# Performance work log

Hardware: AMD Instinct MI355X
Metric: run time of the kernel (lower is better)

## Reference

```python
import jax, jax.numpy as jnp
import numpy as np
from jax import lax

IMG = 256   # model img_size
O = 7       # adaptive pool output size (out_size)
R = 32      # number of ROIs
B = 8       # batch
CF = 32     # UNet output channels
FOUT = 512  # fc out_features


def _conv(x, w, b):
    y = lax.conv_general_dilated(x, w, (1, 1), 'SAME',
                                 dimension_numbers=('NCHW', 'OIHW', 'NCHW'))
    return y + b[None, :, None, None]


def _pool(x):
    return lax.reduce_window(x, -jnp.inf, lax.max, (1, 1, 2, 2), (1, 1, 2, 2), 'VALID')


def _up(x):
    return jnp.repeat(jnp.repeat(x, 2, axis=2), 2, axis=3)


def _unet(x, p):
    r = jax.nn.relu
    e1 = r(_conv(r(_conv(x, p['e1w1'], p['e1b1'])), p['e1w2'], p['e1b2']))          # [B,32,H,W]
    e2 = r(_conv(r(_conv(_pool(e1), p['e2w1'], p['e2b1'])), p['e2w2'], p['e2b2']))  # [B,64,H/2,W/2]
    bo = r(_conv(r(_conv(_pool(e2), p['bw1'], p['bb1'])), p['bw2'], p['bb2']))      # [B,128,H/4,W/4]
    u2 = r(_conv(_up(bo), p['u2w'], p['u2b']))                                      # [B,64,H/2,W/2]
    d2 = r(_conv(r(_conv(jnp.concatenate([u2, e2], 1), p['d2w1'], p['d2b1'])), p['d2w2'], p['d2b2']))
    u1 = r(_conv(_up(d2), p['u1w'], p['u1b']))                                      # [B,32,H,W]
    d1 = r(_conv(r(_conv(jnp.concatenate([u1, e1], 1), p['d1w1'], p['d1b1'])), p['d1w2'], p['d1b2']))
    return _conv(d1, p['fw'], p['fb'])                                              # [B,CF,H,W]


def _adaptive_pool(ii, boxes):
    # Exact F.adaptive_avg_pool2d bins via an integral image.
    # ii: [B,C,H+1,W+1] (zero-padded 2D cumsum); boxes: [R,4] int (x1,y1,x2,y2).
    i = jnp.arange(O)
    h = boxes[:, 3] - boxes[:, 1]
    w = boxes[:, 2] - boxes[:, 0]
    sy = boxes[:, 1:2] + (i[None, :] * h[:, None]) // O            # floor(i*h/O)
    ey = boxes[:, 1:2] + ((i[None, :] + 1) * h[:, None] + O - 1) // O  # ceil((i+1)*h/O)
    sx = boxes[:, 0:1] + (i[None, :] * w[:, None]) // O
    ex = boxes[:, 0:1] + ((i[None, :] + 1) * w[:, None] + O - 1) // O
    yA, yB = sy[:, :, None], ey[:, :, None]   # [R,O,1]
    xA, xB = sx[:, None, :], ex[:, None, :]   # [R,1,O]
    s = ii[:, :, yB, xB] - ii[:, :, yA, xB] - ii[:, :, yB, xA] + ii[:, :, yA, xA]  # [B,C,R,O,O]
    area = ((ey - sy)[:, :, None] * (ex - sx)[:, None, :]).astype(ii.dtype)        # [R,O,O]
    return s / area[None, None]


def _forward(x, rois, p):
    H, W = x.shape[2], x.shape[3]
    xs, ys = IMG // H, IMG // W  # matches torch: x_scale, y_scale = img_size//m, img_size//n
    boxes = rois // jnp.array([xs, ys, xs, ys], dtype=rois.dtype)
    f = _unet(x, p)                                   # [B,CF,H,W]
    ii = jnp.pad(jnp.cumsum(jnp.cumsum(f, axis=2), axis=3),
                 ((0, 0), (0, 0), (1, 0), (1, 0)))    # integral image [B,CF,H+1,W+1]
    rp = _adaptive_pool(ii, boxes)                    # [B,CF,R,O,O]
    roi_feat = jnp.transpose(rp, (0, 2, 1, 3, 4)).reshape(x.shape[0], boxes.shape[0] * f.shape[1], O, O)
    gbox = jnp.array([[0, 0, W, H]], dtype=boxes.dtype)
    gpool = _adaptive_pool(ii, gbox)[:, :, 0]         # [B,CF,O,O]
    out = jnp.concatenate([gpool, roi_feat], axis=1)  # [B,(R+1)*CF,O,O]
    out = out.reshape(out.shape[0], out.shape[1], O * O)
    return jnp.einsum('bnk,fk->bnf', out, p['fcw']) + p['fcb']


_PNAMES = ['e1w1','e1b1','e1w2','e1b2','e2w1','e2b1','e2w2','e2b2','bw1','bb1','bw2','bb2',
           'u2w','u2b','d2w1','d2b1','d2w2','d2b2','u1w','u1b','d1w1','d1b1','d1w2','d1b2',
           'fw','fb','fcw','fcb']


def setup_inputs() -> dict:
    key = jax.random.key(0)
    ks = jax.random.split(key, 32)

    def w(k, shape):
        fan = int(np.prod(shape[1:]))
        return jax.random.normal(k, shape, jnp.float32) * np.sqrt(2.0 / fan)

    d = {}
    d['x'] = jax.random.normal(ks[0], (B, 3, IMG, IMG), jnp.float32)
    xy1 = jax.random.randint(ks[1], (R, 2), 0, 192)
    wh = jax.random.randint(ks[2], (R, 2), 16, 64)
    d['rois'] = jnp.concatenate([xy1, xy1 + wh], axis=1).astype(jnp.int32)  # (x1,y1,x2,y2)

    shapes = {'e1w1': (32, 3, 3, 3), 'e1w2': (32, 32, 3, 3),
              'e2w1': (64, 32, 3, 3), 'e2w2': (64, 64, 3, 3),
              'bw1': (128, 64, 3, 3), 'bw2': (128, 128, 3, 3),
              'u2w': (64, 128, 3, 3),
              'd2w1': (64, 128, 3, 3), 'd2w2': (64, 64, 3, 3),
              'u1w': (32, 64, 3, 3),
              'd1w1': (32, 64, 3, 3), 'd1w2': (32, 32, 3, 3),
              'fw': (CF, 32, 1, 1),
              'fcw': (FOUT, O * O)}
    i = 3
    for n, s in shapes.items():
        d[n] = w(ks[i], s); i += 1
        bn = n.replace('w', 'b', 1) if 'w' in n else n
        d[bn] = jnp.zeros((s[0],), jnp.float32)
    d['fcb'] = jnp.zeros((FOUT,), jnp.float32)
    return d


def reference(x, rois, e1w1, e1b1, e1w2, e1b2, e2w1, e2b1, e2w2, e2b2,
              bw1, bb1, bw2, bb2, u2w, u2b, d2w1, d2b1, d2w2, d2b2,
              u1w, u1b, d1w1, d1b1, d1w2, d1b2, fw, fb, fcw, fcb):
    p = dict(e1w1=e1w1, e1b1=e1b1, e1w2=e1w2, e1b2=e1b2, e2w1=e2w1, e2b1=e2b1,
             e2w2=e2w2, e2b2=e2b2, bw1=bw1, bb1=bb1, bw2=bw2, bb2=bb2,
             u2w=u2w, u2b=u2b, d2w1=d2w1, d2b1=d2b1, d2w2=d2w2, d2b2=d2b2,
             u1w=u1w, u1b=u1b, d1w1=d1w1, d1b1=d1b1, d1w2=d1w2, d1b2=d1b2,
             fw=fw, fb=fb, fcw=fcw, fcb=fcb)
    return _forward(x, rois, p)
```

## Files before the change

### kernel.cpp

```cpp
#include <hip/hip_runtime.h>

typedef _Float16 half8 __attribute__((ext_vector_type(8)));
typedef float f32x4 __attribute__((ext_vector_type(4)));
typedef float f32x16 __attribute__((ext_vector_type(16)));

__device__ __forceinline__ unsigned short f2h(float f) {
    _Float16 h = (_Float16)f;
    return __builtin_bit_cast(unsigned short, h);
}
__device__ __forceinline__ float h2f(unsigned short u) {
    return (float)__builtin_bit_cast(_Float16, u);
}

__device__ __forceinline__ void lds_load16(const uint4* g, uint4* l) {
    __builtin_amdgcn_global_load_lds(
        (const __attribute__((address_space(1))) unsigned int*)g,
        (__attribute__((address_space(3))) unsigned int*)l, 16, 0, 0);
}

#define IIROW 260
#define IIPLANE 66824

__global__ void wprep_k(const float* __restrict__ src, unsigned short* __restrict__ dst,
                        int Cout, int Cin, int total)
{
    int t = blockIdx.x * 256 + threadIdx.x;
    if (t >= total) return;
    int j = t & 7; int r = t >> 3;
    int co = r % Cout; r /= Cout;
    int oct = r & 3; r >>= 2;
    int pos = r % 9; int ck = r / 9;
    int ci = ck * 32 + oct * 8 + j;
    dst[t] = f2h(src[((size_t)co * Cin + ci) * 9 + pos]);
}

__global__ void w1prep_k(const float* __restrict__ src, unsigned short* __restrict__ dst)
{
    int t = blockIdx.x * 256 + threadIdx.x;
    if (t >= 4096) return;
    int j = t & 7, co = (t >> 3) & 31, koct = t >> 8;
    dst[t] = f2h(src[co * 32 + koct * 8 + j]);
}

__global__ void fct_k(const float* __restrict__ src, float* __restrict__ dst)
{
    int t = blockIdx.x * 256 + threadIdx.x;
    if (t >= 49 * 512) return;
    int k = t >> 9, f = t & 511;
    dst[t] = src[f * 49 + k];
}

template<int BM, int TW, int TH, int LW, int UP>
__global__ __launch_bounds__(256, 2) void convm4_k(
    const uint4* __restrict__ in1, int C1g,
    const uint4* __restrict__ in2, int C2g,
    const uint4* __restrict__ wt,
    const float* __restrict__ bias,
    unsigned short* __restrict__ out,
    int Cout, int relu, const uint4* __restrict__ zp)
{
    constexpr int NM = BM / 16;
    constexpr int NN = (TW * TH) / 64;
    constexpr int CG = TW / 16;
    constexpr int RQ = NN / CG;
    static_assert(RQ == 2, "row-reuse layout needs 2 rows/wave");
    constexpr int Wf = 1 << LW, Hf = Wf;
    constexpr int WC = TW + 2, HR = TH + 2;
    constexpr int IN_GR = 4 * HR * WC;
    constexpr int LTW = (TW == 64) ? 6 : 5;
    constexpr int sH = UP ? (Hf >> 1) : Hf;
    constexpr int sW = UP ? (Wf >> 1) : Wf;
    __shared__ uint4 smem[IN_GR + 36 * BM];

    const int tid = threadIdx.x;
    const int lane = tid & 63, wv = tid >> 6;
    const int ng = Cout / BM;
    const int b = blockIdx.z / ng, cg = blockIdx.z % ng;
    const int x0 = blockIdx.x * TW, y0 = blockIdx.y * TH;
    const int NCK = (C1g + C2g) / 4;

    f32x4 acc[NM][NN];
#pragma unroll
    for (int m = 0; m < NM; ++m)
#pragma unroll
        for (int n = 0; n < NN; ++n) acc[m][n] = (f32x4){0.f, 0.f, 0.f, 0.f};

    const int l15 = lane & 15, l4 = lane >> 4;
    const int laneB = l4 * HR * WC + l15;
    const int laneA = l4 * BM + l15;

    for (int ck = 0; ck < NCK; ++ck) {
        if (ck) __syncthreads();
        {
            const uint4* src; int cg0, srcCg;
            if (ck * 4 < C1g) { src = in1; cg0 = ck * 4; srcCg = C1g; }
            else              { src = in2; cg0 = ck * 4 - C1g; srcCg = C2g; }
            for (int i = tid; i < IN_GR; i += 256) {
                int oct = i / (HR * WC);
                int rem = i - oct * (HR * WC);
                int row = rem / WC;
                int col = rem - row * WC;
                int gy = y0 + row - 1, gx = x0 + col - 1;
                int sy = UP ? (gy >> 1) : gy, sx = UP ? (gx >> 1) : gx;
                const uint4* ga = ((unsigned)gy < (unsigned)Hf && (unsigned)gx < (unsigned)Wf)
                    ? src + ((((size_t)b * sH + sy) * sW + sx) * srcCg + cg0 + oct)
                    : zp + (i & 63);
                lds_load16(ga, &smem[i]);
            }
        }
        {
            const uint4* wck = wt + (size_t)ck * 36 * Cout + (size_t)cg * BM;
            for (int i = tid; i < 36 * BM; i += 256) {
                int seg = i / BM, col = i - seg * BM;
                lds_load16(wck + seg * Cout + col, &smem[IN_GR + i]);
            }
        }
        __syncthreads();
        const half8* sB = (const half8*)smem;
        const half8* sA = (const half8*)(smem + IN_GR);
#pragma unroll
        for (int dc = 0; dc < 3; ++dc) {
            half8 br[RQ + 2][CG];
#pragma unroll
            for (int r = 0; r < RQ + 2; ++r)
#pragma unroll
                for (int c2 = 0; c2 < CG; ++c2)
                    br[r][c2] = sB[(wv * RQ + r) * WC + c2 * 16 + dc + laneB];
#pragma unroll
            for (int dr = 0; dr < 3; ++dr) {
                half8 af[NM];
#pragma unroll
                for (int m = 0; m < NM; ++m)
                    af[m] = sA[(dr * 3 + dc) * 4 * BM + m * 16 + laneA];
#pragma unroll
                for (int m = 0; m < NM; ++m)
#pragma unroll
                    for (int rq = 0; rq < RQ; ++rq)
#pragma unroll
                        for (int c2 = 0; c2 < CG; ++c2)
                            acc[m][rq * CG + c2] = __builtin_amdgcn_mfma_f32_16x16x32_f16(
                                af[m], br[rq + dr][c2], acc[m][rq * CG + c2], 0, 0, 0);
            }
        }
    }

#pragma unroll
    for (int m = 0; m < NM; ++m) {
        const int co0 = cg * BM + m * 16 + l4 * 4;
        const float4 bs = *(const float4*)(bias + co0);
#pragma unroll
        for (int n = 0; n < NN; ++n) {
            const int pix = wv * (NN * 16) + n * 16 + l15;
            const int y = y0 + (pix >> LTW), x = x0 + (pix & (TW - 1));
            float v0 = acc[m][n][0] + bs.x;
            float v1 = acc[m][n][1] + bs.y;
            float v2 = acc[m][n][2] + bs.z;
            float v3 = acc[m][n][3] + bs.w;
            if (relu) {
                v0 = fmaxf(v0, 0.f); v1 = fmaxf(v1, 0.f);
                v2 = fmaxf(v2, 0.f); v3 = fmaxf(v3, 0.f);
            }
            uint2 pk;
            pk.x = (unsigned)f2h(v0) | ((unsigned)f2h(v1) << 16);
            pk.y = (unsigned)f2h(v2) | ((unsigned)f2h(v3) << 16);
            *(uint2*)(out + (((size_t)b * Hf + y) * Wf + x) * Cout + co0) = pk;
        }
    }
}

__global__ __launch_bounds__(256) void conv0_k(
    const float* __restrict__ in, const float* __restrict__ w,
    const float* __restrict__ bias, unsigned short* __restrict__ out)
{
    __shared__ float s_in[3][18][18];
    const int tx = threadIdx.x, ty = threadIdx.y;
    const int tid = ty * 16 + tx;
    const int b = blockIdx.z >> 2;
    const int coBase = (blockIdx.z & 3) * 8;
    const int bx = blockIdx.x * 16, by = blockIdx.y * 16;

    for (int i = tid; i < 3 * 18 * 18; i += 256) {
        int cc = i / 324, r = i % 324;
        int ly = r / 18, lx = r % 18;
        int gy = by + ly - 1, gx = bx + lx - 1;
        float v = 0.f;
        if ((unsigned)gy < 256u && (unsigned)gx < 256u)
            v = in[(((size_t)(b * 3 + cc)) << 16) + (gy << 8) + gx];
        ((float*)s_in)[i] = v;
    }
    __syncthreads();
    float acc[8];
#pragma unroll
    for (int k = 0; k < 8; ++k) acc[k] = 0.f;
    for (int cc = 0; cc < 3; ++cc) {
        float v[9];
#pragma unroll
        for (int dh = 0; dh < 3; ++dh)
#pragma unroll
            for (int dw = 0; dw < 3; ++dw)
                v[dh * 3 + dw] = s_in[cc][ty + dh][tx + dw];
        const float* wp = w + ((size_t)coBase * 3 + cc) * 9;
#pragma unroll
        for (int k = 0; k < 8; ++k) {
            const float* wk = wp + (size_t)k * 27;
            float a = acc[k];
#pragma unroll
            for (int j = 0; j < 9; ++j) a = fmaf(v[j], wk[j], a);
            acc[k] = a;
        }
    }
    const int h = by + ty, ww = bx + tx;
    unsigned short* op = out + (((size_t)(b * 256 + h)) * 256 + ww) * 32 + coBase;
#pragma unroll
    for (int k = 0; k < 8; ++k)
        op[k] = f2h(fmaxf(acc[k] + bias[coBase + k], 0.f));
}

__global__ void poolh_k(const uint4* __restrict__ in, uint4* __restrict__ out,
                        int Ho, int Wo, int C8, int total)
{
    int i = blockIdx.x * 256 + threadIdx.x;
    if (i >= total) return;
    int oct = i % C8; int p = i / C8;
    int x = p % Wo; p /= Wo;
    int y = p % Ho; int b = p / Ho;
    const int H = Ho * 2, W = Wo * 2;
    size_t g = (((size_t)b * H + 2 * y) * W + 2 * x) * C8 + oct;
    uint4 v00 = in[g], v01 = in[g + C8];
    uint4 v10 = in[g + (size_t)W * C8], v11 = in[g + (size_t)W * C8 + C8];
    const unsigned short* a0 = (const unsigned short*)&v00;
    const unsigned short* a1 = (const unsigned short*)&v01;
    const unsigned short* a2 = (const unsigned short*)&v10;
    const unsigned short* a3 = (const unsigned short*)&v11;
    uint4 res; unsigned short* rp = (unsigned short*)&res;
#pragma unroll
    for (int j = 0; j < 8; ++j)
        rp[j] = f2h(fmaxf(fmaxf(h2f(a0[j]), h2f(a1[j])), fmaxf(h2f(a2[j]), h2f(a3[j]))));
    out[(((size_t)b * Ho + y) * Wo + x) * C8 + oct] = res;
}

__global__ __launch_bounds__(256) void rowprep_k(
    const uint4* __restrict__ in, const uint4* __restrict__ w16,
    const float* __restrict__ bias, float* __restrict__ ii)
{
    __shared__ uint4 sIn[1024];
    __shared__ uint4 sW[128];
    __shared__ float sout[32][256];
    __shared__ float sb[32];
    const int tid = threadIdx.x;
    const int lane = tid & 63, wv = tid >> 6;
    const int l31 = lane & 31, l5 = lane >> 5;
    const int y = blockIdx.x, b = blockIdx.y;

    const uint4* ip = in + (((size_t)b * 256 + y) * 256) * 4;
#pragma unroll
    for (int it = 0; it < 4; ++it)
        lds_load16(ip + tid + it * 256, &sIn[tid + it * 256]);
    if (tid < 128) lds_load16(w16 + tid, &sW[tid]);
    if (tid < 32) sb[tid] = bias[tid];
    __syncthreads();

    const half8* hW = (const half8*)sW;
    const half8* hIn = (const half8*)sIn;
    half8 af0 = hW[l5 * 32 + l31];
    half8 af1 = hW[(2 + l5) * 32 + l31];
#pragma unroll
    for (int g = 0; g < 2; ++g) {
        const int p0 = wv * 64 + g * 32;
        half8 bf0 = hIn[(p0 + l31) * 4 + l5];
        half8 bf1 = hIn[(p0 + l31) * 4 + 2 + l5];
        f32x16 acc;
#pragma unroll
        for (int q = 0; q < 16; ++q) acc[q] = 0.f;
        acc = __builtin_amdgcn_mfma_f32_32x32x16_f16(af0, bf0, acc, 0, 0, 0);
        acc = __builtin_amdgcn_mfma_f32_32x32x16_f16(af1, bf1, acc, 0, 0, 0);
#pragma unroll
        for (int r = 0; r < 16; ++r) {
            const int co = (r & 3) + 8 * (r >> 2) + 4 * l5;
            sout[co][p0 + l31] = acc[r] + sb[co];
        }
    }
    __syncthreads();

    float* plane0 = ii + (size_t)(b * 32) * IIPLANE;
    if (y == 0) {
        for (int i = tid; i < 32 * 257; i += 256) {
            int c = i / 257, xx = i % 257;
            plane0[(size_t)c * IIPLANE + xx + 3] = 0.f;
        }
    }
    for (int cc = 0; cc < 8; ++cc) {
        const int c = wv * 8 + cc;
        float* prow = plane0 + (size_t)c * IIPLANE + (size_t)(y + 1) * IIROW;
        float4 v = *(const float4*)&sout[c][lane * 4];
        float s0 = v.x, s1 = s0 + v.y, s2 = s1 + v.z, s3 = s2 + v.w;
        float t = s3;
#pragma unroll
        for (int off = 1; off < 64; off <<= 1) {
            float u = __shfl_up(t, off);
            if (lane >= off) t += u;
        }
        const float base = t - s3;
        float4 o;
        o.x = base + s0; o.y = base + s1; o.z = base + s2; o.w = base + s3;
        *(float4*)(prow + 4 + lane * 4) = o;
        if (lane == 0) prow[3] = 0.f;
    }
}

__global__ __launch_bounds__(256) void colA_k(const float* __restrict__ ii,
                                              float* __restrict__ S)
{
    const int p = blockIdx.x, s = blockIdx.y;
    const int x = threadIdx.x;
    const float* plane = ii + (size_t)p * IIPLANE;
    float acc = 0.f;
#pragma unroll 8
    for (int y = s * 64 + 1; y <= s * 64 + 64; ++y)
        acc += plane[(size_t)y * IIROW + x + 4];
    S[(p * 3 + s) * 256 + x] = acc;
}

__global__ __launch_bounds__(256) void colB_k(float* __restrict__ ii,
                                              const float* __restrict__ S)
{
    const int p = blockIdx.x, s = blockIdx.y;
    const int x = threadIdx.x;
    float* plane = ii + (size_t)p * IIPLANE;
    float acc = 0.f;
    for (int t = 0; t < s; ++t) acc += S[(p * 3 + t) * 256 + x];
#pragma unroll 8
    for (int y = s * 64 + 1; y <= s * 64 + 64; ++y) {
        float* q = plane + (size_t)y * IIROW + x + 4;
        acc += *q;
        *q = acc;
    }
}

__global__ void pool_k(const float* __restrict__ ii, const int* __restrict__ rois,
                       float* __restrict__ pooled)
{
    int t = blockIdx.x * 256 + threadIdx.x;
    int k = t % 49; int nb = t / 49;
    int n = nb % 1056; int b = nb / 1056;
    int ki = k / 7, kj = k % 7;
    int x1, y1, x2, y2, c;
    if (n < 32) {
        x1 = 0; y1 = 0; x2 = 256; y2 = 256; c = n;
    } else {
        int r = (n - 32) >> 5;
        c = (n - 32) & 31;
        x1 = rois[r * 4 + 0]; y1 = rois[r * 4 + 1];
        x2 = rois[r * 4 + 2]; y2 = rois[r * 4 + 3];
    }
    const int h = y2 - y1, w = x2 - x1;
    const int sy = y1 + (ki * h) / 7, ey = y1 + ((ki + 1) * h + 6) / 7;
    const int sx = x1 + (kj * w) / 7, ex = x1 + ((kj + 1) * w + 6) / 7;
    const float* pl = ii + (size_t)(b * 32 + c) * IIPLANE + 3;
    float s = pl[ey * IIROW + ex] - pl[sy * IIROW + ex]
            - pl[ey * IIROW + sx] + pl[sy * IIROW + sx];
    pooled[t] = s / (float)((ey - sy) * (ex - sx));
}

__global__ __launch_bounds__(512) void fc_k(
    const float* __restrict__ pooled, const float* __restrict__ fcwT,
    const float* __restrict__ fcb, float* __restrict__ out)
{
    const int nt = blockIdx.x, b = blockIdx.y;
    const int f = threadIdx.x;
    float wr[49];
#pragma unroll
    for (int k = 0; k < 49; ++k) wr[k] = fcwT[k * 512 + f];
    const float base = fcb[f];
    const float* pr = pooled + ((size_t)b * 1056 + nt * 16) * 49;
    float* op = out + (((size_t)b * 1056 + nt * 16)) * 512 + f;
#pragma unroll
    for (int j = 0; j < 16; ++j) {
        float a = base;
#pragma unroll
        for (int k = 0; k < 49; ++k)
            a = fmaf(pr[j * 49 + k], wr[k], a);
        op[(size_t)j * 512] = a;
    }
}

extern "C" void kernel_launch(void* const* d_in, const int* in_sizes, int n_in,
                              void* d_out, int out_size, void* d_ws, size_t ws_size,
                              hipStream_t stream)
{
    const float* x    = (const float*)d_in[0];
    const int*   rois = (const int*)d_in[1];
    const float* e1w1 = (const float*)d_in[2];
    const float* e1b1 = (const float*)d_in[3];
    const float* e1w2 = (const float*)d_in[4];
    const float* e1b2 = (const float*)d_in[5];
    const float* e2w1 = (const float*)d_in[6];
    const float* e2b1 = (const float*)d_in[7];
    const float* e2w2 = (const float*)d_in[8];
    const float* e2b2 = (const float*)d_in[9];
    const float* bw1  = (const float*)d_in[10];
    const float* bb1  = (const float*)d_in[11];
    const float* bw2  = (const float*)d_in[12];
    const float* bb2  = (const float*)d_in[13];
    const float* u2w  = (const float*)d_in[14];
    const float* u2b  = (const float*)d_in[15];
    const float* d2w1 = (const float*)d_in[16];
    const float* d2b1 = (const float*)d_in[17];
    const float* d2w2 = (const float*)d_in[18];
    const float* d2b2 = (const float*)d_in[19];
    const float* u1w  = (const float*)d_in[20];
    const float* u1b  = (const float*)d_in[21];
    const float* d1w1 = (const float*)d_in[22];
    const float* d1b1 = (const float*)d_in[23];
    const float* d1w2 = (const float*)d_in[24];
    const float* d1b2 = (const float*)d_in[25];
    const float* fw   = (const float*)d_in[26];
    const float* fb   = (const float*)d_in[27];
    const float* fcw  = (const float*)d_in[28];
    const float* fcb  = (const float*)d_in[29];

    char* wsb = (char*)d_ws;
    char* WT = wsb;
    char* A  = wsb + 4194304;
    char* D  = A + 33554432;
    char* E  = D + 16777216;
    char* Bb = E + 16777216;
    char* C  = Bb + 33554432;
    char* F  = C + 8388608;
    float* ii     = (float*)F;
    float* fcwT   = (float*)(WT + 1179648);
    unsigned short* fw16 = (unsigned short*)(WT + 2097152);
    uint4* zp     = (uint4*)(WT + 4194304 - 8192);
    float* pooled = (float*)C;
    float* Sbuf   = (float*)(C + 2097152);
    hipMemsetAsync(zp, 0, 8192, stream);

    const float* wsrc[11] = {e1w2, e2w1, e2w2, bw1, bw2, u2w, d2w1, d2w2, u1w, d1w1, d1w2};
    const int wco[11] = {32, 64, 64, 128, 128, 64, 64, 64, 32, 32, 32};
    const int wci[11] = {32, 32, 64, 64, 128, 128, 128, 64, 64, 64, 32};
    size_t woff[11]; size_t o = 0;
    for (int i = 0; i < 11; ++i) { woff[i] = o; o += (size_t)wco[i] * wci[i] * 18; }
    for (int i = 0; i < 11; ++i) {
        int total = wco[i] * wci[i] * 9;
        hipLaunchKernelGGL(wprep_k, dim3((total + 255) / 256), dim3(256), 0, stream,
                           wsrc[i], (unsigned short*)(WT + woff[i]), wco[i], wci[i], total);
    }
    hipLaunchKernelGGL(fct_k, dim3((49 * 512 + 255) / 256), dim3(256), 0, stream, fcw, fcwT);
    hipLaunchKernelGGL(w1prep_k, dim3(16), dim3(256), 0, stream, fw, fw16);
    auto WP = [&](int i) { return (const uint4*)(WT + woff[i]); };

    #define CV1(i1,C1,i2,C2,wi,bs,ot,Cout,up,rl) \
        hipLaunchKernelGGL((convm4_k<32,64,8,8,up>), dim3(4,32,8*((Cout)/32)), dim3(256), 0, stream, \
            (const uint4*)(i1), (C1)/8, (const uint4*)(i2), (C2)/8, WP(wi), bs, \
            (unsigned short*)(ot), Cout, rl, zp)
    #define CV2(i1,C1,i2,C2,wi,bs,ot,Cout,up,rl) \
        hipLaunchKernelGGL((convm4_k<64,32,8,7,up>), dim3(4,16,8*((Cout)/64)), dim3(256), 0, stream, \
            (const uint4*)(i1), (C1)/8, (const uint4*)(i2), (C2)/8, WP(wi), bs, \
            (unsigned short*)(ot), Cout, rl, zp)
    #define CV3(i1,C1,i2,C2,wi,bs,ot,Cout,up,rl) \
        hipLaunchKernelGGL((convm4_k<32,32,8,6,up>), dim3(2,8,8*((Cout)/32)), dim3(256), 0, stream, \
            (const uint4*)(i1), (C1)/8, (const uint4*)(i2), (C2)/8, WP(wi), bs, \
            (unsigned short*)(ot), Cout, rl, zp)

    hipLaunchKernelGGL(conv0_k, dim3(16, 16, 32), dim3(16, 16), 0, stream,
                       x, e1w1, e1b1, (unsigned short*)A);
    CV1(A, 32, nullptr, 0, 0, e1b2, Bb, 32, 0, 1);
    {
        int N = 8 * 128 * 128 * 4;
        hipLaunchKernelGGL(poolh_k, dim3((N + 255) / 256), dim3(256), 0, stream,
                           (const uint4*)Bb, (uint4*)C, 128, 128, 4, N);
    }
    CV2(C, 32, nullptr, 0, 1, e2b1, A, 64, 0, 1);
    CV2(A, 64, nullptr, 0, 2, e2b2, D, 64, 0, 1);
    {
        int N = 8 * 64 * 64 * 8;
        hipLaunchKernelGGL(poolh_k, dim3((N + 255) / 256), dim3(256), 0, stream,
                           (const uint4*)D, (uint4*)C, 64, 64, 8, N);
    }
    CV3(C, 64, nullptr, 0, 3, bb1, E, 128, 0, 1);
    CV3(E, 128, nullptr, 0, 4, bb2, A, 128, 0, 1);
    CV2(A, 128, nullptr, 0, 5, u2b, E, 64, 1, 1);
    CV2(E, 64, D, 64, 6, d2b1, A, 64, 0, 1);
    CV2(A, 64, nullptr, 0, 7, d2b2, D, 64, 0, 1);
    CV1(D, 64, nullptr, 0, 8, u1b, A, 32, 1, 1);
    CV1(A, 32, Bb, 32, 9, d1b1, D, 32, 0, 1);
    CV1(D, 32, nullptr, 0, 10, d1b2, Bb, 32, 0, 1);
    hipLaunchKernelGGL(rowprep_k, dim3(256, 8), dim3(256), 0, stream,
                       (const uint4*)Bb, (const uint4*)fw16, fb, ii);
    hipLaunchKernelGGL(colA_k, dim3(256, 3), dim3(256), 0, stream, ii, Sbuf);
    hipLaunchKernelGGL(colB_k, dim3(256, 4), dim3(256), 0, stream, ii, Sbuf);
    hipLaunchKernelGGL(pool_k, dim3(8 * 1056 * 49 / 256), dim3(256), 0, stream,
                       ii, rois, pooled);
    hipLaunchKernelGGL(fc_k, dim3(66, 8), dim3(512), 0, stream,
                       pooled, fcwT, fcb, (float*)d_out);
    #undef CV1
    #undef CV2
    #undef CV3
}
```

Measured before the change: 397.5 us.

## Replace integral-image ROI pooling with direct fp16 bin summation and merge weight-prep launches

The 1x1 final conv now writes an fp16 feature map instead of building row-scanned fp32 integral images, and the two column-scan kernels are removed. A new pooling kernel, one block per (batch, ROI-channel), sums each adaptive bin directly over the fp16 map. This avoids writing and rescanning the large fp32 integral-image buffer. In exchange, each thread runs a long serial loop of scalar loads and extra fp16 rounding enters the averages. Separately, the eleven weight-prep launches plus the fc-transpose and 1x1-weight prep are merged into a single kernel driven by an offset table, to cut launch overhead.

```diff
diff --git a/kernel.cpp b/kernel.cpp
--- a/kernel.cpp
+++ b/kernel.cpp
@@ -18,36 +18,37 @@
         (__attribute__((address_space(3))) unsigned int*)l, 16, 0, 0);
 }
 
-#define IIROW 260
-#define IIPLANE 66824
-
-__global__ void wprep_k(const float* __restrict__ src, unsigned short* __restrict__ dst,
-                        int Cout, int Cin, int total)
-{
-    int t = blockIdx.x * 256 + threadIdx.x;
-    if (t >= total) return;
-    int j = t & 7; int r = t >> 3;
-    int co = r % Cout; r /= Cout;
-    int oct = r & 3; r >>= 2;
-    int pos = r % 9; int ck = r / 9;
-    int ci = ck * 32 + oct * 8 + j;
-    dst[t] = f2h(src[((size_t)co * Cin + ci) * 9 + pos]);
-}
-
-__global__ void w1prep_k(const float* __restrict__ src, unsigned short* __restrict__ dst)
-{
-    int t = blockIdx.x * 256 + threadIdx.x;
-    if (t >= 4096) return;
-    int j = t & 7, co = (t >> 3) & 31, koct = t >> 8;
-    dst[t] = f2h(src[co * 32 + koct * 8 + j]);
-}
-
-__global__ void fct_k(const float* __restrict__ src, float* __restrict__ dst)
-{
-    int t = blockIdx.x * 256 + threadIdx.x;
-    if (t >= 49 * 512) return;
-    int k = t >> 9, f = t & 511;
-    dst[t] = src[f * 49 + k];
+struct PrepArgs {
+    const float* src[13];
+    unsigned dstOff[13];
+    int Cout[13], Cin[13];
+    unsigned off[14];
+};
+
+__global__ void prep_all_k(PrepArgs a, char* __restrict__ WT)
+{
+    unsigned t = blockIdx.x * 256 + threadIdx.x;
+    if (t >= a.off[13]) return;
+    int l = 0;
+    while (t >= a.off[l + 1]) ++l;
+    unsigned e = t - a.off[l];
+    if (l < 11) {
+        int j = e & 7; unsigned r = e >> 3;
+        const int Cout = a.Cout[l], Cin = a.Cin[l];
+        int co = r % Cout; r /= Cout;
+        int oct = r & 3; r >>= 2;
+        int pos = r % 9; int ck = r / 9;
+        int ci = ck * 32 + oct * 8 + j;
+        ((unsigned short*)(WT + a.dstOff[l]))[e] =
+            f2h(a.src[l][((size_t)co * Cin + ci) * 9 + pos]);
+    } else if (l == 11) {
+        int k = e >> 9, ff = e & 511;
+        ((float*)(WT + a.dstOff[l]))[e] = a.src[l][ff * 49 + k];
+    } else {
+        int j = e & 7, co = (e >> 3) & 31, koct = e >> 8;
+        ((unsigned short*)(WT + a.dstOff[l]))[e] =
+            f2h(a.src[l][co * 32 + koct * 8 + j]);
+    }
 }
 
 template<int BM, int TW, int TH, int LW, int UP>
@@ -239,13 +240,12 @@
     out[(((size_t)b * Ho + y) * Wo + x) * C8 + oct] = res;
 }
 
-__global__ __launch_bounds__(256) void rowprep_k(
+__global__ __launch_bounds__(256) void conv1x1f_k(
     const uint4* __restrict__ in, const uint4* __restrict__ w16,
-    const float* __restrict__ bias, float* __restrict__ ii)
+    const float* __restrict__ bias, unsigned short* __restrict__ f)
 {
     __shared__ uint4 sIn[1024];
     __shared__ uint4 sW[128];
-    __shared__ float sout[32][256];
     __shared__ float sb[32];
     const int tid = threadIdx.x;
     const int lane = tid & 63, wv = tid >> 6;
@@ -264,6 +264,7 @@
     const half8* hIn = (const half8*)sIn;
     half8 af0 = hW[l5 * 32 + l31];
     half8 af1 = hW[(2 + l5) * 32 + l31];
+    unsigned short* fp_ = f + ((size_t)b * 32) * 65536 + (size_t)y * 256;
 #pragma unroll
     for (int g = 0; g < 2; ++g) {
         const int p0 = wv * 64 + g * 32;
@@ -277,73 +278,19 @@
 #pragma unroll
         for (int r = 0; r < 16; ++r) {
             const int co = (r & 3) + 8 * (r >> 2) + 4 * l5;
-            sout[co][p0 + l31] = acc[r] + sb[co];
-        }
-    }
-    __syncthreads();
-
-    float* plane0 = ii + (size_t)(b * 32) * IIPLANE;
-    if (y == 0) {
-        for (int i = tid; i < 32 * 257; i += 256) {
-            int c = i / 257, xx = i % 257;
-            plane0[(size_t)c * IIPLANE + xx + 3] = 0.f;
-        }
-    }
-    for (int cc = 0; cc < 8; ++cc) {
-        const int c = wv * 8 + cc;
-        float* prow = plane0 + (size_t)c * IIPLANE + (size_t)(y + 1) * IIROW;
-        float4 v = *(const float4*)&sout[c][lane * 4];
-        float s0 = v.x, s1 = s0 + v.y, s2 = s1 + v.z, s3 = s2 + v.w;
-        float t = s3;
-#pragma unroll
-        for (int off = 1; off < 64; off <<= 1) {
-            float u = __shfl_up(t, off);
-            if (lane >= off) t += u;
-        }
-        const float base = t - s3;
-        float4 o;
-        o.x = base + s0; o.y = base + s1; o.z = base + s2; o.w = base + s3;
-        *(float4*)(prow + 4 + lane * 4) = o;
-        if (lane == 0) prow[3] = 0.f;
-    }
-}
-
-__global__ __launch_bounds__(256) void colA_k(const float* __restrict__ ii,
-                                              float* __restrict__ S)
-{
-    const int p = blockIdx.x, s = blockIdx.y;
-    const int x = threadIdx.x;
-    const float* plane = ii + (size_t)p * IIPLANE;
-    float acc = 0.f;
-#pragma unroll 8
-    for (int y = s * 64 + 1; y <= s * 64 + 64; ++y)
-        acc += plane[(size_t)y * IIROW + x + 4];
-    S[(p * 3 + s) * 256 + x] = acc;
-}
-
-__global__ __launch_bounds__(256) void colB_k(float* __restrict__ ii,
-                                              const float* __restrict__ S)
-{
-    const int p = blockIdx.x, s = blockIdx.y;
-    const int x = threadIdx.x;
-    float* plane = ii + (size_t)p * IIPLANE;
-    float acc = 0.f;
-    for (int t = 0; t < s; ++t) acc += S[(p * 3 + t) * 256 + x];
-#pragma unroll 8
-    for (int y = s * 64 + 1; y <= s * 64 + 64; ++y) {
-        float* q = plane + (size_t)y * IIROW + x + 4;
-        acc += *q;
-        *q = acc;
-    }
-}
-
-__global__ void pool_k(const float* __restrict__ ii, const int* __restrict__ rois,
-                       float* __restrict__ pooled)
-{
-    int t = blockIdx.x * 256 + threadIdx.x;
-    int k = t % 49; int nb = t / 49;
-    int n = nb % 1056; int b = nb / 1056;
-    int ki = k / 7, kj = k % 7;
+            fp_[(size_t)co * 65536 + p0 + l31] = f2h(acc[r] + sb[co]);
+        }
+    }
+}
+
+__global__ __launch_bounds__(64) void poold_k(
+    const unsigned short* __restrict__ f, const int* __restrict__ rois,
+    float* __restrict__ pooled)
+{
+    const int n = blockIdx.x, b = blockIdx.y;
+    const int k = threadIdx.x;
+    if (k >= 49) return;
+    const int ki = k / 7, kj = k % 7;
     int x1, y1, x2, y2, c;
     if (n < 32) {
         x1 = 0; y1 = 0; x2 = 256; y2 = 256; c = n;
@@ -356,10 +303,13 @@
     const int h = y2 - y1, w = x2 - x1;
     const int sy = y1 + (ki * h) / 7, ey = y1 + ((ki + 1) * h + 6) / 7;
     const int sx = x1 + (kj * w) / 7, ex = x1 + ((kj + 1) * w + 6) / 7;
-    const float* pl = ii + (size_t)(b * 32 + c) * IIPLANE + 3;
-    float s = pl[ey * IIROW + ex] - pl[sy * IIROW + ex]
-            - pl[ey * IIROW + sx] + pl[sy * IIROW + sx];
-    pooled[t] = s / (float)((ey - sy) * (ex - sx));
+    const unsigned short* pl = f + (size_t)(b * 32 + c) * 65536;
+    float s = 0.f;
+    for (int y = sy; y < ey; ++y) {
+        const unsigned short* row = pl + (size_t)y * 256;
+        for (int x = sx; x < ex; ++x) s += h2f(row[x]);
+    }
+    pooled[((size_t)b * 1056 + n) * 49 + k] = s / (float)((ey - sy) * (ex - sx));
 }
 
 __global__ __launch_bounds__(512) void fc_k(
@@ -427,26 +377,31 @@
     char* Bb = E + 16777216;
     char* C  = Bb + 33554432;
     char* F  = C + 8388608;
-    float* ii     = (float*)F;
     float* fcwT   = (float*)(WT + 1179648);
     unsigned short* fw16 = (unsigned short*)(WT + 2097152);
     uint4* zp     = (uint4*)(WT + 4194304 - 8192);
+    unsigned short* fpl = (unsigned short*)F;
     float* pooled = (float*)C;
-    float* Sbuf   = (float*)(C + 2097152);
     hipMemsetAsync(zp, 0, 8192, stream);
 
     const float* wsrc[11] = {e1w2, e2w1, e2w2, bw1, bw2, u2w, d2w1, d2w2, u1w, d1w1, d1w2};
     const int wco[11] = {32, 64, 64, 128, 128, 64, 64, 64, 32, 32, 32};
     const int wci[11] = {32, 32, 64, 64, 128, 128, 128, 64, 64, 64, 32};
     size_t woff[11]; size_t o = 0;
-    for (int i = 0; i < 11; ++i) { woff[i] = o; o += (size_t)wco[i] * wci[i] * 18; }
+    PrepArgs pa;
+    unsigned eoff = 0;
     for (int i = 0; i < 11; ++i) {
-        int total = wco[i] * wci[i] * 9;
-        hipLaunchKernelGGL(wprep_k, dim3((total + 255) / 256), dim3(256), 0, stream,
-                           wsrc[i], (unsigned short*)(WT + woff[i]), wco[i], wci[i], total);
-    }
-    hipLaunchKernelGGL(fct_k, dim3((49 * 512 + 255) / 256), dim3(256), 0, stream, fcw, fcwT);
-    hipLaunchKernelGGL(w1prep_k, dim3(16), dim3(256), 0, stream, fw, fw16);
+        woff[i] = o; o += (size_t)wco[i] * wci[i] * 18;
+        pa.src[i] = wsrc[i]; pa.dstOff[i] = (unsigned)woff[i];
+        pa.Cout[i] = wco[i]; pa.Cin[i] = wci[i];
+        pa.off[i] = eoff; eoff += (unsigned)(wco[i] * wci[i] * 9);
+    }
+    pa.src[11] = fcw; pa.dstOff[11] = 1179648; pa.Cout[11] = 0; pa.Cin[11] = 0;
+    pa.off[11] = eoff; eoff += 49 * 512;
+    pa.src[12] = fw; pa.dstOff[12] = 2097152; pa.Cout[12] = 0; pa.Cin[12] = 0;
+    pa.off[12] = eoff; eoff += 4096;
+    pa.off[13] = eoff;
+    hipLaunchKernelGGL(prep_all_k, dim3((eoff + 255) / 256), dim3(256), 0, stream, pa, WT);
     auto WP = [&](int i) { return (const uint4*)(WT + woff[i]); };
 
     #define CV1(i1,C1,i2,C2,wi,bs,ot,Cout,up,rl) \
@@ -485,12 +440,10 @@
     CV1(D, 64, nullptr, 0, 8, u1b, A, 32, 1, 1);
     CV1(A, 32, Bb, 32, 9, d1b1, D, 32, 0, 1);
     CV1(D, 32, nullptr, 0, 10, d1b2, Bb, 32, 0, 1);
-    hipLaunchKernelGGL(rowprep_k, dim3(256, 8), dim3(256), 0, stream,
-                       (const uint4*)Bb, (const uint4*)fw16, fb, ii);
-    hipLaunchKernelGGL(colA_k, dim3(256, 3), dim3(256), 0, stream, ii, Sbuf);
-    hipLaunchKernelGGL(colB_k, dim3(256, 4), dim3(256), 0, stream, ii, Sbuf);
-    hipLaunchKernelGGL(pool_k, dim3(8 * 1056 * 49 / 256), dim3(256), 0, stream,
-                       ii, rois, pooled);
+    hipLaunchKernelGGL(conv1x1f_k, dim3(256, 8), dim3(256), 0, stream,
+                       (const uint4*)Bb, (const uint4*)fw16, fb, fpl);
+    hipLaunchKernelGGL(poold_k, dim3(1056, 8), dim3(64), 0, stream,
+                       fpl, rois, pooled);
     hipLaunchKernelGGL(fc_k, dim3(66, 8), dim3(512), 0, stream,
                        pooled, fcwT, fcb, (float*)d_out);
     #undef CV1
```

Measured after the change: 456.4 us. 14.8% more time.
